# Kernel tuning notes

Hardware: AMD Instinct MI355X
Metric: run time of the kernel (lower is better)

The kernel has to match this reference:

```python
import jax, jax.numpy as jnp
import numpy as np

N = 20000
E = 320000
NEG_SLOPE = 0.2
BN_EPS = 1e-5


def _segment_softmax(e, dst, n):
    # e: [E, H] attention logits, dst: [E] destination node ids
    m = jax.ops.segment_max(e, dst, num_segments=n)           # [N, H]
    ex = jnp.exp(e - m[dst])                                   # [E, H]
    s = jax.ops.segment_sum(ex, dst, num_segments=n)          # [N, H]
    return ex / s[dst]


def gat_conv(x, src, dst, W, a_src, a_dst, b, heads, out_ch):
    # PyG GATConv (concat=True): h = x @ W reshaped to [N, H, C]
    n = x.shape[0]
    h = (x @ W).reshape(n, heads, out_ch)                      # [N, H, C]
    al_s = jnp.einsum('nhc,hc->nh', h, a_src)                  # [N, H]
    al_d = jnp.einsum('nhc,hc->nh', h, a_dst)
    e = jax.nn.leaky_relu(al_s[src] + al_d[dst], NEG_SLOPE)    # [E, H]
    alpha = _segment_softmax(e, dst, n)                        # [E, H]
    msg = h[src] * alpha[:, :, None]                           # [E, H, C]
    out = jax.ops.segment_sum(msg, dst, num_segments=n)        # [N, H, C]
    return out.reshape(n, heads * out_ch) + b


def batch_norm(x, gamma, beta):
    mu = jnp.mean(x, axis=0)
    var = jnp.mean((x - mu) ** 2, axis=0)  # biased, as torch BN training
    return gamma * (x - mu) * jax.lax.rsqrt(var + BN_EPS) + beta


def setup_inputs() -> dict:
    key = jax.random.key(0)
    ks = jax.random.split(key, 16)
    F_in, H1, C1 = 128, 8, 64
    D = H1 * C1  # 512
    OUT = 2
    def gl(k, shape, fan):
        return jax.random.normal(k, shape, dtype=jnp.float32) / np.sqrt(fan)
    x = jax.random.normal(ks[0], (N, F_in), dtype=jnp.float32)
    edge_index = jax.random.randint(ks[1], (2, E), 0, N, dtype=jnp.int64)
    return {
        'x': x, 'edge_index': edge_index,
        'W1': gl(ks[2], (F_in, H1 * C1), F_in),
        'a1s': gl(ks[3], (H1, C1), C1), 'a1d': gl(ks[4], (H1, C1), C1),
        'b1': jnp.zeros((D,), jnp.float32),
        'W2': gl(ks[5], (D, D), D),
        'a2s': gl(ks[6], (1, D), D), 'a2d': gl(ks[7], (1, D), D),
        'b2': jnp.zeros((D,), jnp.float32),
        'fc1_w': gl(ks[8], (D, D), D), 'fc1_b': jnp.zeros((D,), jnp.float32),
        'g1': jnp.ones((D,), jnp.float32), 'be1': jnp.zeros((D,), jnp.float32),
        'fc2_w': gl(ks[9], (D, D), D), 'fc2_b': jnp.zeros((D,), jnp.float32),
        'g2': jnp.ones((D,), jnp.float32), 'be2': jnp.zeros((D,), jnp.float32),
        'lin_w': gl(ks[10], (D, OUT), D), 'lin_b': jnp.zeros((OUT,), jnp.float32),
    }


def reference(x, edge_index, W1, a1s, a1d, b1, W2, a2s, a2d, b2,
              fc1_w, fc1_b, g1, be1, fc2_w, fc2_b, g2, be2, lin_w, lin_b):
    n = x.shape[0]
    loop = jnp.arange(n, dtype=edge_index.dtype)
    src = jnp.concatenate([edge_index[0], loop])  # add self-loops (PyG default)
    dst = jnp.concatenate([edge_index[1], loop])
    h = gat_conv(x, src, dst, W1, a1s, a1d, b1, heads=8, out_ch=64)
    h = batch_norm(jax.nn.relu(h @ fc1_w + fc1_b), g1, be1)
    h = gat_conv(h, src, dst, W2, a2s, a2d, b2, heads=1, out_ch=512)
    h = batch_norm(jax.nn.relu(h @ fc2_w + fc2_b), g2, be2)
    out = jax.nn.relu(h @ lin_w + lin_b)  # dropout p=0 is identity
    return out
```

## Files before the change

kernel.cpp:

```cpp
#include <hip/hip_runtime.h>
#include <hip/hip_bf16.h>

static constexpr int NN = 20000;
static constexpr int EE = 320000;
static constexpr int ET = EE + NN;
static constexpr int DD = 512;
static constexpr int FIN = 128;

typedef __attribute__((ext_vector_type(8))) short short8;
typedef __attribute__((ext_vector_type(4))) float f32x4;

__device__ __forceinline__ unsigned short f2bf(float f) {
    unsigned u = __float_as_uint(f);
    u += 0x7fffu + ((u >> 16) & 1u);
    return (unsigned short)(u >> 16);
}
__device__ __forceinline__ float bf2f(unsigned short b) {
    return __uint_as_float(((unsigned)b) << 16);
}

__device__ __forceinline__ void async_copy16(short* lds, const unsigned short* g) {
    __builtin_amdgcn_global_load_lds(
        (const __attribute__((address_space(1))) unsigned int*)g,
        (__attribute__((address_space(3))) unsigned int*)lds,
        16, 0, 0);
}

__global__ void detect_idx64(const unsigned* __restrict__ ei, int* __restrict__ flag) {
    int is64 = 1;
    for (int i = 0; i < 64; ++i)
        if (ei[2 * i + 1] != 0u) { is64 = 0; break; }
    *flag = is64;
}

__global__ void init_deg_cursor(int* __restrict__ deg, int* __restrict__ cursor) {
    int i = blockIdx.x * blockDim.x + threadIdx.x;
    if (i < NN) { deg[i] = 1; cursor[i] = 0; }
}

__global__ void convert_idx(const void* __restrict__ ei, const int* __restrict__ flag,
                            int* __restrict__ src32, int* __restrict__ dst32,
                            int* __restrict__ deg) {
    int i = blockIdx.x * blockDim.x + threadIdx.x;
    if (i >= EE) return;
    int s, d;
    if (*flag) {
        const long long* p = (const long long*)ei;
        s = (int)p[i]; d = (int)p[EE + i];
    } else {
        const int* p = (const int*)ei;
        s = p[i]; d = p[EE + i];
    }
    src32[i] = s;
    dst32[i] = d;
    atomicAdd(&deg[d], 1);
}

__global__ void scan_k(const int* __restrict__ deg, int* __restrict__ row_ptr) {
    __shared__ int part[1024];
    int t = threadIdx.x;
    const int CH = (NN + 1023) / 1024;
    int start = t * CH;
    int end = min(start + CH, NN);
    int s = 0;
    for (int i = start; i < end; ++i) s += deg[i];
    part[t] = s;
    __syncthreads();
    for (int off = 1; off < 1024; off <<= 1) {
        int v = 0;
        if (t >= off) v = part[t - off];
        __syncthreads();
        part[t] += v;
        __syncthreads();
    }
    int base = (t == 0) ? 0 : part[t - 1];
    for (int i = start; i < end; ++i) { row_ptr[i] = base; base += deg[i]; }
    if (t == 1023) row_ptr[NN] = part[1023];
}

__global__ void fill_csr(const int* __restrict__ src, const int* __restrict__ dst,
                         const int* __restrict__ row_ptr, int* __restrict__ cursor,
                         int* __restrict__ csr_src) {
    int e = blockIdx.x * blockDim.x + threadIdx.x;
    if (e >= ET) return;
    int d = (e < EE) ? dst[e] : (e - EE);
    int s = (e < EE) ? src[e] : (e - EE);
    int pos = atomicAdd(&cursor[d], 1);
    csr_src[row_ptr[d] + pos] = s;
}

static constexpr int SZ_X  = NN * FIN;
static constexpr int SZ_W1 = FIN * DD;
static constexpr int SZ_W  = DD * DD;
static constexpr int SZ_Z  = 2 * 1024 + 2 * NN;
__global__ void prep_k(const float* __restrict__ x, const float* __restrict__ W1,
                       const float* __restrict__ fc1, const float* __restrict__ W2,
                       const float* __restrict__ fc2,
                       unsigned short* __restrict__ xb, unsigned short* __restrict__ W1t,
                       unsigned short* __restrict__ fc1t, unsigned short* __restrict__ W2t,
                       unsigned short* __restrict__ fc2t,
                       float* __restrict__ bnstatA, float* __restrict__ bnstatB,
                       float* __restrict__ al_s2, float* __restrict__ al_d2) {
    int i = blockIdx.x * blockDim.x + threadIdx.x;
    if (i < SZ_X) { xb[i] = f2bf(x[i]); return; }
    i -= SZ_X;
    if (i < SZ_W1) {
        int k = i / DD, n = i - k * DD;
        W1t[(size_t)n * FIN + k] = f2bf(W1[i]);
        return;
    }
    i -= SZ_W1;
    if (i < 3 * SZ_W) {
        const float* Wp; unsigned short* Tp;
        if (i < SZ_W) { Wp = fc1; Tp = fc1t; }
        else if (i < 2 * SZ_W) { i -= SZ_W; Wp = W2; Tp = W2t; }
        else { i -= 2 * SZ_W; Wp = fc2; Tp = fc2t; }
        int k = i / DD, n = i - k * DD;
        Tp[(size_t)n * DD + k] = f2bf(Wp[i]);
        return;
    }
    i -= 3 * SZ_W;
    if (i < 1024) { bnstatA[i] = 0.f; return; }
    i -= 1024;
    if (i < 1024) { bnstatB[i] = 0.f; return; }
    i -= 1024;
    if (i < NN) { al_s2[i] = 0.f; return; }
    i -= NN;
    if (i < NN) { al_d2[i] = 0.f; return; }
}

template <int RELU, int HASBIAS, int OUTBF, int STATS, int ALS, int H>
__global__ __launch_bounds__(256) void gemm_bf16(const unsigned short* __restrict__ A,
                                                 const unsigned short* __restrict__ Bt,
                                                 const float* __restrict__ bias,
                                                 float* __restrict__ C,
                                                 unsigned short* __restrict__ Cb,
                                                 float* __restrict__ bnstat,
                                                 const float* __restrict__ avs,
                                                 const float* __restrict__ avd,
                                                 float* __restrict__ al_s,
                                                 float* __restrict__ al_d,
                                                 int M, int Nc, int K) {
    __shared__ short As0[128 * 32], As1[128 * 32];
    __shared__ short Bs0[128 * 32], Bs1[128 * 32];
    int t = threadIdx.x;
    int m0 = blockIdx.y * 128, n0 = blockIdx.x * 128;
    int lane = t & 63, w = t >> 6;
    int wm = w & 1, wn = w >> 1;
    int quad = lane >> 4, mr = lane & 15;
    int lrow = lane >> 2;
    int lcol = (lane & 3) * 8;

    const unsigned short* Ag0 = A + (size_t)(m0 + w * 32 + lrow) * K + lcol;
    const unsigned short* Ag1 = A + (size_t)(m0 + w * 32 + 16 + lrow) * K + lcol;
    const unsigned short* Bg0 = Bt + (size_t)(n0 + w * 32 + lrow) * K + lcol;
    const unsigned short* Bg1 = Bt + (size_t)(n0 + w * 32 + 16 + lrow) * K + lcol;
    short* Al[2][2] = {{&As0[(w * 32) * 32], &As0[(w * 32 + 16) * 32]},
                       {&As1[(w * 32) * 32], &As1[(w * 32 + 16) * 32]}};
    short* Bl[2][2] = {{&Bs0[(w * 32) * 32], &Bs0[(w * 32 + 16) * 32]},
                       {&Bs1[(w * 32) * 32], &Bs1[(w * 32 + 16) * 32]}};

    f32x4 zero = {0.f, 0.f, 0.f, 0.f};
    f32x4 acc[4][4];
#pragma unroll
    for (int i = 0; i < 4; ++i)
#pragma unroll
        for (int j = 0; j < 4; ++j) acc[i][j] = zero;

    for (int k0 = 0; k0 < K; k0 += 64) {
        async_copy16(Al[0][0], Ag0 + k0);
        async_copy16(Al[1][0], Ag0 + k0 + 32);
        async_copy16(Al[0][1], Ag1 + k0);
        async_copy16(Al[1][1], Ag1 + k0 + 32);
        async_copy16(Bl[0][0], Bg0 + k0);
        async_copy16(Bl[1][0], Bg0 + k0 + 32);
        async_copy16(Bl[0][1], Bg1 + k0);
        async_copy16(Bl[1][1], Bg1 + k0 + 32);
        __syncthreads();
#pragma unroll
        for (int kp = 0; kp < 2; ++kp) {
            const short* Sa = kp ? As1 : As0;
            const short* Sb = kp ? Bs1 : Bs0;
            short8 af[4], bfr[4];
#pragma unroll
            for (int i = 0; i < 4; ++i) {
                af[i]  = *(const short8*)(&Sa[(wm * 64 + i * 16 + mr) * 32 + quad * 8]);
                bfr[i] = *(const short8*)(&Sb[(wn * 64 + i * 16 + mr) * 32 + quad * 8]);
            }
#pragma unroll
            for (int i = 0; i < 4; ++i)
#pragma unroll
                for (int j = 0; j < 4; ++j)
                    acc[i][j] = __builtin_amdgcn_mfma_f32_16x16x32_bf16(af[i], bfr[j], acc[i][j], 0, 0, 0);
        }
        __syncthreads();
    }

    float as_j[4], ad_j[4];
    if (ALS) {
#pragma unroll
        for (int j = 0; j < 4; ++j) {
            int n = n0 + wn * 64 + j * 16 + mr;
            as_j[j] = avs[n];
            ad_j[j] = avd[n];
        }
    }
    const int head = (H == 8) ? ((n0 + wn * 64) >> 6) : 0;
    float sj[4] = {0.f, 0.f, 0.f, 0.f}, qj[4] = {0.f, 0.f, 0.f, 0.f};
#pragma unroll
    for (int i = 0; i < 4; ++i) {
        int mb = m0 + wm * 64 + i * 16 + quad * 4;
#pragma unroll
        for (int r = 0; r < 4; ++r) {
            int m = mb + r;
            bool valid = (m < M);
            float ps = 0.f, pd = 0.f;
#pragma unroll
            for (int j = 0; j < 4; ++j) {
                int n = n0 + wn * 64 + j * 16 + mr;
                float v = acc[i][j][r];
                if (HASBIAS) v += bias[n];
                if (RELU) v = fmaxf(v, 0.f);
                if (OUTBF) {
                    unsigned short hb = f2bf(v);
                    if (valid) Cb[(size_t)m * Nc + n] = hb;
                    if (ALS) {
                        float vv = bf2f(hb);
                        ps += as_j[j] * vv;
                        pd += ad_j[j] * vv;
                    }
                } else {
                    if (valid) C[(size_t)m * Nc + n] = v;
                }
                if (STATS && valid) { sj[j] += v; qj[j] += v * v; }
            }
            if (ALS) {
                ps += __shfl_xor(ps, 1); pd += __shfl_xor(pd, 1);
                ps += __shfl_xor(ps, 2); pd += __shfl_xor(pd, 2);
                ps += __shfl_xor(ps, 4); pd += __shfl_xor(pd, 4);
                ps += __shfl_xor(ps, 8); pd += __shfl_xor(pd, 8);
                if (mr == 0 && valid) {
                    if (H == 8) { al_s[m * 8 + head] = ps; al_d[m * 8 + head] = pd; }
                    else        { atomicAdd(&al_s[m], ps); atomicAdd(&al_d[m], pd); }
                }
            }
        }
    }
    if (STATS) {
#pragma unroll
        for (int j = 0; j < 4; ++j) {
            float s = sj[j], q = qj[j];
            s += __shfl_xor(s, 16); q += __shfl_xor(q, 16);
            s += __shfl_xor(s, 32); q += __shfl_xor(q, 32);
            if (lane < 16) {
                int n = n0 + wn * 64 + j * 16 + mr;
                atomicAdd(&bnstat[n], s);
                atomicAdd(&bnstat[512 + n], q);
            }
        }
    }
}

template <int H>
__global__ __launch_bounds__(256) void gat_gather_k(const unsigned short* __restrict__ hb,
                                                    const float* __restrict__ al_s,
                                                    const float* __restrict__ al_d,
                                                    const int* __restrict__ row_ptr,
                                                    const int* __restrict__ csr_src,
                                                    const float* __restrict__ bias,
                                                    unsigned short* __restrict__ outb) {
    int t = threadIdx.x;
    int w = t >> 6, lane = t & 63;
    int n = blockIdx.x * 4 + w;
    int beg = row_ptr[n], end = row_ptr[n + 1];
    const int hh = (H == 8) ? (lane >> 3) : 0;
    float ald = al_d[n * H + hh];
    float psum = 0.f;
    float acc[8] = {0.f, 0.f, 0.f, 0.f, 0.f, 0.f, 0.f, 0.f};

    for (int p0 = beg; p0 < end; p0 += 64) {
        int cnt = min(64, end - p0);
        int sv = (p0 + lane < end) ? csr_src[p0 + lane] : 0;
        int p = 0;
        for (; p + 8 <= cnt; p += 8) {
            int sn[8];
#pragma unroll
            for (int u = 0; u < 8; ++u) sn[u] = __shfl(sv, p + u);
            float l[8];
#pragma unroll
            for (int u = 0; u < 8; ++u) l[u] = al_s[sn[u] * H + hh] + ald;
            short8 hv[8];
#pragma unroll
            for (int u = 0; u < 8; ++u)
                hv[u] = *(const short8*)(hb + (size_t)sn[u] * DD + lane * 8);
            float a[8];
#pragma unroll
            for (int u = 0; u < 8; ++u) {
                float x = l[u];
                a[u] = __expf((x > 0.f) ? x : 0.2f * x);
                psum += a[u];
            }
#pragma unroll
            for (int u = 0; u < 8; ++u)
#pragma unroll
                for (int j = 0; j < 8; ++j) acc[j] += a[u] * bf2f((unsigned short)hv[u][j]);
        }
        for (; p < cnt; ++p) {
            int sn0 = __shfl(sv, p);
            float l0 = al_s[sn0 * H + hh] + ald;
            short8 h0 = *(const short8*)(hb + (size_t)sn0 * DD + lane * 8);
            float a0 = __expf((l0 > 0.f) ? l0 : 0.2f * l0);
            psum += a0;
#pragma unroll
            for (int j = 0; j < 8; ++j) acc[j] += a0 * bf2f((unsigned short)h0[j]);
        }
    }
    float inv = 1.0f / psum;
    unsigned short ov[8];
#pragma unroll
    for (int j = 0; j < 8; ++j) ov[j] = f2bf(acc[j] * inv + bias[lane * 8 + j]);
    *(int4*)(outb + (size_t)n * DD + lane * 8) = *(const int4*)ov;
}

__global__ void bn_apply1(float* __restrict__ x, const float* __restrict__ stat,
                          const float* __restrict__ g, const float* __restrict__ be,
                          unsigned short* __restrict__ xb) {
    int i = (blockIdx.x * blockDim.x + threadIdx.x) * 4;
    int c = i & (DD - 1);
    float4 v = *(const float4*)(x + i);
    float o[4];
    float* vp = &v.x;
#pragma unroll
    for (int j = 0; j < 4; ++j) {
        int cc = c + j;
        float mean = stat[cc] * (1.0f / NN);
        float var = stat[512 + cc] * (1.0f / NN) - mean * mean;
        float sc = g[cc] * rsqrtf(var + 1e-5f);
        o[j] = (vp[j] - mean) * sc + be[cc];
    }
    ushort4 ob;
    ob.x = f2bf(o[0]); ob.y = f2bf(o[1]); ob.z = f2bf(o[2]); ob.w = f2bf(o[3]);
    *(ushort4*)(xb + i) = ob;
}

__global__ void fold_k(const float* __restrict__ stat, const float* __restrict__ g,
                       const float* __restrict__ be, const float* __restrict__ w,
                       const float* __restrict__ b, float* __restrict__ wfold,
                       float* __restrict__ bfold) {
    __shared__ float r0[512], r1[512];
    int c = threadIdx.x;
    float mean = stat[c] * (1.0f / NN);
    float var = stat[512 + c] * (1.0f / NN) - mean * mean;
    float sc = g[c] * rsqrtf(var + 1e-5f);
    float sh = be[c] - mean * sc;
    float w0 = w[2 * c], w1 = w[2 * c + 1];
    wfold[2 * c] = sc * w0;
    wfold[2 * c + 1] = sc * w1;
    r0[c] = sh * w0;
    r1[c] = sh * w1;
    __syncthreads();
    for (int off = 256; off; off >>= 1) {
        if (c < off) { r0[c] += r0[c + off]; r1[c] += r1[c + off]; }
        __syncthreads();
    }
    if (c == 0) { bfold[0] = r0[0] + b[0]; bfold[1] = r1[0] + b[1]; }
}

__global__ void final_linear(const float* __restrict__ x, const float* __restrict__ w,
                             const float* __restrict__ b, float* __restrict__ out) {
    int wave = (blockIdx.x * blockDim.x + threadIdx.x) >> 6;
    int lane = threadIdx.x & 63;
    if (wave >= NN) return;
    const float* row = x + (size_t)wave * DD;
    float p0 = 0.f, p1 = 0.f;
    for (int c = lane; c < DD; c += 64) {
        float v = row[c];
        p0 += v * w[2 * c];
        p1 += v * w[2 * c + 1];
    }
    for (int off = 32; off; off >>= 1) {
        p0 += __shfl_down(p0, off);
        p1 += __shfl_down(p1, off);
    }
    if (lane == 0) {
        out[wave * 2 + 0] = fmaxf(p0 + b[0], 0.f);
        out[wave * 2 + 1] = fmaxf(p1 + b[1], 0.f);
    }
}

extern "C" void kernel_launch(void* const* d_in, const int* in_sizes, int n_in,
                              void* d_out, int out_size, void* d_ws, size_t ws_size,
                              hipStream_t stream) {
    const float* x     = (const float*)d_in[0];
    const void*  ei    = d_in[1];
    const float* W1    = (const float*)d_in[2];
    const float* a1s   = (const float*)d_in[3];
    const float* a1d   = (const float*)d_in[4];
    const float* b1    = (const float*)d_in[5];
    const float* W2    = (const float*)d_in[6];
    const float* a2s   = (const float*)d_in[7];
    const float* a2d   = (const float*)d_in[8];
    const float* b2    = (const float*)d_in[9];
    const float* fc1_w = (const float*)d_in[10];
    const float* fc1_b = (const float*)d_in[11];
    const float* g1    = (const float*)d_in[12];
    const float* be1   = (const float*)d_in[13];
    const float* fc2_w = (const float*)d_in[14];
    const float* fc2_b = (const float*)d_in[15];
    const float* g2    = (const float*)d_in[16];
    const float* be2   = (const float*)d_in[17];
    const float* lin_w = (const float*)d_in[18];
    const float* lin_b = (const float*)d_in[19];
    float* out = (float*)d_out;

    char* ws = (char*)d_ws;
    auto alloc = [&](size_t bytes) {
        void* p = (void*)ws;
        ws += (bytes + 255) & ~size_t(255);
        return p;
    };
    float*          bufC    = (float*)alloc((size_t)NN * DD * 4);
    unsigned short* h_bf    = (unsigned short*)alloc((size_t)NN * DD * 2);
    unsigned short* act_bf  = (unsigned short*)alloc((size_t)NN * DD * 2);
    unsigned short* W1t     = (unsigned short*)alloc((size_t)DD * FIN * 2);
    unsigned short* fc1t    = (unsigned short*)alloc((size_t)DD * DD * 2);
    unsigned short* W2t     = (unsigned short*)alloc((size_t)DD * DD * 2);
    unsigned short* fc2t    = (unsigned short*)alloc((size_t)DD * DD * 2);
    float*          al_s    = (float*)alloc((size_t)NN * 8 * 4);
    float*          al_d    = (float*)alloc((size_t)NN * 8 * 4);
    float*          al_s2   = (float*)alloc((size_t)NN * 4);
    float*          al_d2   = (float*)alloc((size_t)NN * 4);
    int*            row_ptr = (int*)alloc((size_t)(NN + 1) * 4);
    int*            deg     = (int*)alloc((size_t)NN * 4);
    int*            cursor  = (int*)alloc((size_t)NN * 4);
    int*            csr_src = (int*)alloc((size_t)ET * 4);
    int*            src32   = (int*)alloc((size_t)EE * 4);
    int*            dst32   = (int*)alloc((size_t)EE * 4);
    int*            flag    = (int*)alloc(256);
    float*          bnstatA = (float*)alloc(1024 * 4);
    float*          bnstatB = (float*)alloc(1024 * 4);
    float*          wfold   = (float*)alloc(1024 * 4);
    float*          bfold   = (float*)alloc(256);

    detect_idx64<<<1, 1, 0, stream>>>((const unsigned*)ei, flag);
    init_deg_cursor<<<(NN + 255) / 256, 256, 0, stream>>>(deg, cursor);
    convert_idx<<<(EE + 255) / 256, 256, 0, stream>>>(ei, flag, src32, dst32, deg);
    scan_k<<<1, 1024, 0, stream>>>(deg, row_ptr);
    fill_csr<<<(ET + 255) / 256, 256, 0, stream>>>(src32, dst32, row_ptr, cursor, csr_src);

    unsigned short* x_bf = act_bf;
    const int prep_total = SZ_X + SZ_W1 + 3 * SZ_W + SZ_Z;
    prep_k<<<(prep_total + 255) / 256, 256, 0, stream>>>(x, W1, fc1_w, W2, fc2_w,
                                                         x_bf, W1t, fc1t, W2t, fc2t,
                                                         bnstatA, bnstatB, al_s2, al_d2);

    dim3 gg(DD / 128, (NN + 127) / 128);

    gemm_bf16<0, 0, 1, 0, 1, 8><<<gg, 256, 0, stream>>>(
        x_bf, W1t, nullptr, nullptr, h_bf, nullptr, a1s, a1d, al_s, al_d, NN, DD, FIN);
    gat_gather_k<8><<<NN / 4, 256, 0, stream>>>(h_bf, al_s, al_d, row_ptr, csr_src, b1, act_bf);
    gemm_bf16<1, 1, 0, 1, 0, 8><<<gg, 256, 0, stream>>>(
        act_bf, fc1t, fc1_b, bufC, nullptr, bnstatA, nullptr, nullptr, nullptr, nullptr, NN, DD, DD);
    bn_apply1<<<(NN * DD / 4) / 256, 256, 0, stream>>>(bufC, bnstatA, g1, be1, act_bf);

    gemm_bf16<0, 0, 1, 0, 1, 1><<<gg, 256, 0, stream>>>(
        act_bf, W2t, nullptr, nullptr, h_bf, nullptr, a2s, a2d, al_s2, al_d2, NN, DD, DD);
    gat_gather_k<1><<<NN / 4, 256, 0, stream>>>(h_bf, al_s2, al_d2, row_ptr, csr_src, b2, act_bf);
    gemm_bf16<1, 1, 0, 1, 0, 8><<<gg, 256, 0, stream>>>(
        act_bf, fc2t, fc2_b, bufC, nullptr, bnstatB, nullptr, nullptr, nullptr, nullptr, NN, DD, DD);

    fold_k<<<1, 512, 0, stream>>>(bnstatB, g2, be2, lin_w, lin_b, wfold, bfold);
    final_linear<<<(NN + 3) / 4, 256, 0, stream>>>(bufC, wfold, bfold, out);
}
```

Baseline: 390.0 us.

## Fold first batchnorm into W2 weights and store GEMM outputs as bf16

Removes the bn_apply1 pass by folding the first batch-norm scale into the W2 weight columns and its shift into a new per-column bias computed by a small kernel. The fc GEMMs now write bf16 instead of fp32, so the final linear reads bf16 rows, which halves those memory writes and reads. The index-width detection is merged into the init kernel to save a launch. The cost is an extra bf16 rounding of the scaled weights and of the pre-BN activations, which may change numerics slightly.

```diff
diff --git a/kernel.cpp b/kernel.cpp
--- a/kernel.cpp
+++ b/kernel.cpp
@@ -26,16 +26,16 @@
         16, 0, 0);
 }
 
-__global__ void detect_idx64(const unsigned* __restrict__ ei, int* __restrict__ flag) {
-    int is64 = 1;
-    for (int i = 0; i < 64; ++i)
-        if (ei[2 * i + 1] != 0u) { is64 = 0; break; }
-    *flag = is64;
-}
-
-__global__ void init_deg_cursor(int* __restrict__ deg, int* __restrict__ cursor) {
+__global__ void init_k(int* __restrict__ deg, int* __restrict__ cursor,
+                       const unsigned* __restrict__ ei, int* __restrict__ flag) {
     int i = blockIdx.x * blockDim.x + threadIdx.x;
     if (i < NN) { deg[i] = 1; cursor[i] = 0; }
+    if (i == 0) {
+        int is64 = 1;
+        for (int j = 0; j < 64; ++j)
+            if (ei[2 * j + 1] != 0u) { is64 = 0; break; }
+        *flag = is64;
+    }
 }
 
 __global__ void convert_idx(const void* __restrict__ ei, const int* __restrict__ flag,
@@ -129,11 +129,10 @@
     if (i < NN) { al_d2[i] = 0.f; return; }
 }
 
-template <int RELU, int HASBIAS, int OUTBF, int STATS, int ALS, int H>
+template <int RELU, int HASBIAS, int STATS, int ALS, int H>
 __global__ __launch_bounds__(256) void gemm_bf16(const unsigned short* __restrict__ A,
                                                  const unsigned short* __restrict__ Bt,
                                                  const float* __restrict__ bias,
-                                                 float* __restrict__ C,
                                                  unsigned short* __restrict__ Cb,
                                                  float* __restrict__ bnstat,
                                                  const float* __restrict__ avs,
@@ -221,16 +220,12 @@
                 float v = acc[i][j][r];
                 if (HASBIAS) v += bias[n];
                 if (RELU) v = fmaxf(v, 0.f);
-                if (OUTBF) {
-                    unsigned short hb = f2bf(v);
-                    if (valid) Cb[(size_t)m * Nc + n] = hb;
-                    if (ALS) {
-                        float vv = bf2f(hb);
-                        ps += as_j[j] * vv;
-                        pd += ad_j[j] * vv;
-                    }
-                } else {
-                    if (valid) C[(size_t)m * Nc + n] = v;
+                unsigned short hb = f2bf(v);
+                if (valid) Cb[(size_t)m * Nc + n] = hb;
+                if (ALS) {
+                    float vv = bf2f(hb);
+                    ps += as_j[j] * vv;
+                    pd += ad_j[j] * vv;
                 }
                 if (STATS && valid) { sj[j] += v; qj[j] += v * v; }
             }
@@ -322,25 +317,28 @@
     *(int4*)(outb + (size_t)n * DD + lane * 8) = *(const int4*)ov;
 }
 
-__global__ void bn_apply1(float* __restrict__ x, const float* __restrict__ stat,
-                          const float* __restrict__ g, const float* __restrict__ be,
-                          unsigned short* __restrict__ xb) {
-    int i = (blockIdx.x * blockDim.x + threadIdx.x) * 4;
-    int c = i & (DD - 1);
-    float4 v = *(const float4*)(x + i);
-    float o[4];
-    float* vp = &v.x;
-#pragma unroll
-    for (int j = 0; j < 4; ++j) {
-        int cc = c + j;
-        float mean = stat[cc] * (1.0f / NN);
-        float var = stat[512 + cc] * (1.0f / NN) - mean * mean;
-        float sc = g[cc] * rsqrtf(var + 1e-5f);
-        o[j] = (vp[j] - mean) * sc + be[cc];
-    }
-    ushort4 ob;
-    ob.x = f2bf(o[0]); ob.y = f2bf(o[1]); ob.z = f2bf(o[2]); ob.w = f2bf(o[3]);
-    *(ushort4*)(xb + i) = ob;
+__global__ __launch_bounds__(256) void fold1_k(const float* __restrict__ stat,
+                                               const float* __restrict__ g,
+                                               const float* __restrict__ be,
+                                               unsigned short* __restrict__ W2t,
+                                               float* __restrict__ bias2) {
+    int t = threadIdx.x;
+    int n = blockIdx.x * 4 + (t >> 6);
+    int lane = t & 63;
+    float pb = 0.f;
+#pragma unroll
+    for (int j = 0; j < 8; ++j) {
+        int k = lane * 8 + j;
+        float mean = stat[k] * (1.0f / NN);
+        float var = stat[512 + k] * (1.0f / NN) - mean * mean;
+        float sc = g[k] * rsqrtf(var + 1e-5f);
+        float sh = be[k] - mean * sc;
+        float wv = bf2f(W2t[n * DD + k]);
+        W2t[n * DD + k] = f2bf(sc * wv);
+        pb += sh * wv;
+    }
+    for (int off = 32; off; off >>= 1) pb += __shfl_down(pb, off);
+    if (lane == 0) bias2[n] = pb;
 }
 
 __global__ void fold_k(const float* __restrict__ stat, const float* __restrict__ g,
@@ -366,15 +364,17 @@
     if (c == 0) { bfold[0] = r0[0] + b[0]; bfold[1] = r1[0] + b[1]; }
 }
 
-__global__ void final_linear(const float* __restrict__ x, const float* __restrict__ w,
+__global__ void final_linear(const unsigned short* __restrict__ xb, const float* __restrict__ w,
                              const float* __restrict__ b, float* __restrict__ out) {
     int wave = (blockIdx.x * blockDim.x + threadIdx.x) >> 6;
     int lane = threadIdx.x & 63;
     if (wave >= NN) return;
-    const float* row = x + (size_t)wave * DD;
+    short8 hv = *(const short8*)(xb + (size_t)wave * DD + lane * 8);
     float p0 = 0.f, p1 = 0.f;
-    for (int c = lane; c < DD; c += 64) {
-        float v = row[c];
+#pragma unroll
+    for (int j = 0; j < 8; ++j) {
+        int c = lane * 8 + j;
+        float v = bf2f((unsigned short)hv[j]);
         p0 += v * w[2 * c];
         p1 += v * w[2 * c + 1];
     }
@@ -419,7 +419,6 @@
         ws += (bytes + 255) & ~size_t(255);
         return p;
     };
-    float*          bufC    = (float*)alloc((size_t)NN * DD * 4);
     unsigned short* h_bf    = (unsigned short*)alloc((size_t)NN * DD * 2);
     unsigned short* act_bf  = (unsigned short*)alloc((size_t)NN * DD * 2);
     unsigned short* W1t     = (unsigned short*)alloc((size_t)DD * FIN * 2);
@@ -439,11 +438,11 @@
     int*            flag    = (int*)alloc(256);
     float*          bnstatA = (float*)alloc(1024 * 4);
     float*          bnstatB = (float*)alloc(1024 * 4);
+    float*          bias2f  = (float*)alloc(512 * 4);
     float*          wfold   = (float*)alloc(1024 * 4);
     float*          bfold   = (float*)alloc(256);
 
-    detect_idx64<<<1, 1, 0, stream>>>((const unsigned*)ei, flag);
-    init_deg_cursor<<<(NN + 255) / 256, 256, 0, stream>>>(deg, cursor);
+    init_k<<<(NN + 255) / 256, 256, 0, stream>>>(deg, cursor, (const unsigned*)ei, flag);
     convert_idx<<<(EE + 255) / 256, 256, 0, stream>>>(ei, flag, src32, dst32, deg);
     scan_k<<<1, 1024, 0, stream>>>(deg, row_ptr);
     fill_csr<<<(ET + 255) / 256, 256, 0, stream>>>(src32, dst32, row_ptr, cursor, csr_src);
@@ -456,19 +455,19 @@
 
     dim3 gg(DD / 128, (NN + 127) / 128);
 
-    gemm_bf16<0, 0, 1, 0, 1, 8><<<gg, 256, 0, stream>>>(
-        x_bf, W1t, nullptr, nullptr, h_bf, nullptr, a1s, a1d, al_s, al_d, NN, DD, FIN);
+    gemm_bf16<0, 0, 0, 1, 8><<<gg, 256, 0, stream>>>(
+        x_bf, W1t, nullptr, h_bf, nullptr, a1s, a1d, al_s, al_d, NN, DD, FIN);
     gat_gather_k<8><<<NN / 4, 256, 0, stream>>>(h_bf, al_s, al_d, row_ptr, csr_src, b1, act_bf);
-    gemm_bf16<1, 1, 0, 1, 0, 8><<<gg, 256, 0, stream>>>(
-        act_bf, fc1t, fc1_b, bufC, nullptr, bnstatA, nullptr, nullptr, nullptr, nullptr, NN, DD, DD);
-    bn_apply1<<<(NN * DD / 4) / 256, 256, 0, stream>>>(bufC, bnstatA, g1, be1, act_bf);
-
-    gemm_bf16<0, 0, 1, 0, 1, 1><<<gg, 256, 0, stream>>>(
-        act_bf, W2t, nullptr, nullptr, h_bf, nullptr, a2s, a2d, al_s2, al_d2, NN, DD, DD);
-    gat_gather_k<1><<<NN / 4, 256, 0, stream>>>(h_bf, al_s2, al_d2, row_ptr, csr_src, b2, act_bf);
-    gemm_bf16<1, 1, 0, 1, 0, 8><<<gg, 256, 0, stream>>>(
-        act_bf, fc2t, fc2_b, bufC, nullptr, bnstatB, nullptr, nullptr, nullptr, nullptr, NN, DD, DD);
+    gemm_bf16<1, 1, 1, 0, 8><<<gg, 256, 0, stream>>>(
+        act_bf, fc1t, fc1_b, h_bf, bnstatA, nullptr, nullptr, nullptr, nullptr, NN, DD, DD);
+    fold1_k<<<128, 256, 0, stream>>>(bnstatA, g1, be1, W2t, bias2f);
+
+    gemm_bf16<0, 1, 0, 1, 1><<<gg, 256, 0, stream>>>(
+        h_bf, W2t, bias2f, act_bf, nullptr, a2s, a2d, al_s2, al_d2, NN, DD, DD);
+    gat_gather_k<1><<<NN / 4, 256, 0, stream>>>(act_bf, al_s2, al_d2, row_ptr, csr_src, b2, h_bf);
+    gemm_bf16<1, 1, 1, 0, 8><<<gg, 256, 0, stream>>>(
+        h_bf, fc2t, fc2_b, act_bf, bnstatB, nullptr, nullptr, nullptr, nullptr, NN, DD, DD);
 
     fold_k<<<1, 512, 0, stream>>>(bnstatB, g2, be2, lin_w, lin_b, wfold, bfold);
-    final_linear<<<(NN + 3) / 4, 256, 0, stream>>>(bufC, wfold, bfold, out);
-}
+    final_linear<<<(NN + 3) / 4, 256, 0, stream>>>(act_bf, wfold, bfold, out);
+}
```

Result: faster. 375.3 us (-3.8%).
